# Kernel tuning notes

Measured on AMD Instinct MI355X. Metric: run time of the kernel, lower is better.

## Reference

```python
import jax, jax.numpy as jnp
import numpy as np

NEG_INF = -1e30


def setup_inputs() -> dict:
    key = jax.random.key(0)
    k1, k2, k3, k4 = jax.random.split(key, 4)
    B, T, C, H = 4, 4096, 1024, 64
    x = jax.random.normal(k1, (B, T, C), dtype=jnp.float32)
    Wk = jax.random.normal(k2, (C, H), dtype=jnp.float32) * (C ** -0.5)
    Wq = jax.random.normal(k3, (C, H), dtype=jnp.float32) * (C ** -0.5)
    Wv = jax.random.normal(k4, (C, H), dtype=jnp.float32) * (C ** -0.5)
    return {"x": x, "Wk": Wk, "Wq": Wq, "Wv": Wv}


def reference(x, Wk, Wq, Wv):
    # x: [B, T, C]; Wq/Wk/Wv: [C, H]
    B, T, C = x.shape
    q = jnp.einsum('btc,ch->bth', x, Wq)  # [B,T,H]
    k = jnp.einsum('btc,ch->bth', x, Wk)  # [B,T,H]
    v = jnp.einsum('btc,ch->bth', x, Wv)  # [B,T,H]
    # NOTE: original scales by C**-0.5 (n_embd), not head_size**-0.5.
    scale = jnp.asarray(C, x.dtype) ** -0.5
    wei = jnp.einsum('bth,bsh->bts', q, k) * scale  # [B,T,T]
    causal = jnp.tril(jnp.ones((T, T), dtype=bool))
    wei = jnp.where(causal, wei, NEG_INF)
    wei = jax.nn.softmax(wei, axis=-1)
    # dropout p=0.0 -> identity
    out = jnp.einsum('bts,bsh->bth', wei, v)  # [B,T,H]
    return out
```

## Files before the change

kernel.cpp:

```cpp
#include <hip/hip_runtime.h>
#include <math.h>

typedef short bfx8 __attribute__((ext_vector_type(8)));
typedef short bfx4 __attribute__((ext_vector_type(4)));
typedef float fx4  __attribute__((ext_vector_type(4)));

__device__ __forceinline__ unsigned short f2bf(float f) {
    unsigned int u = __builtin_bit_cast(unsigned int, f);
    u += 0x7FFFu + ((u >> 16) & 1u);
    return (unsigned short)(u >> 16);
}

__global__ __launch_bounds__(256) void wt_prep(const float* __restrict__ Wq,
                                               const float* __restrict__ Wk,
                                               const float* __restrict__ Wv,
                                               unsigned short* __restrict__ wt)
{
    const int k0  = blockIdx.x * 64;
    const int mat = blockIdx.y;
    const float* W = (mat == 0) ? Wq : ((mat == 1) ? Wk : Wv);
    const float scale = (mat == 0) ? 0.03125f : 1.0f;
    __shared__ unsigned short Ls[64 * 68];
    const int t = threadIdx.x;
    #pragma unroll
    for (int i = 0; i < 4; ++i) {
        int idx4 = t + 256 * i;
        int r = idx4 >> 4, c4 = idx4 & 15;
        float4 v = *(const float4*)&W[(size_t)(k0 + r) * 64 + c4 * 4];
        Ls[r * 68 + c4 * 4 + 0] = f2bf(v.x * scale);
        Ls[r * 68 + c4 * 4 + 1] = f2bf(v.y * scale);
        Ls[r * 68 + c4 * 4 + 2] = f2bf(v.z * scale);
        Ls[r * 68 + c4 * 4 + 3] = f2bf(v.w * scale);
    }
    __syncthreads();
    #pragma unroll
    for (int i = 0; i < 2; ++i) {
        int u = t + 256 * i;
        int n = u >> 3, kc = u & 7;
        bfx8 o;
        #pragma unroll
        for (int j = 0; j < 8; ++j) o[j] = (short)Ls[(kc * 8 + j) * 68 + n];
        *(bfx8*)&wt[(size_t)(mat * 64 + n) * 1024 + k0 + kc * 8] = o;
    }
}

__global__ __launch_bounds__(256) void qkv_mfma(
    const float* __restrict__ x, const unsigned short* __restrict__ wt,
    unsigned short* __restrict__ qb, unsigned short* __restrict__ kb,
    unsigned short* __restrict__ vt)
{
    __shared__ alignas(16) char smem[65536];
    const int t = threadIdx.x;
    const int w = t >> 6, l = t & 63, g = l >> 4, li = l & 15;
    const int m0 = blockIdx.x * 64;

    fx4 acc[12];
    #pragma unroll
    for (int i = 0; i < 12; ++i) acc[i] = (fx4){0.f, 0.f, 0.f, 0.f};

    float4 xr[4]; bfx8 wr[6];

#define QKV_LOAD(K0) do { \
    _Pragma("unroll") for (int i_ = 0; i_ < 4; ++i_) { int idx4 = t + 256 * i_; int r_ = idx4 >> 4, c4 = idx4 & 15; \
        xr[i_] = *(const float4*)&x[(size_t)(m0 + r_) * 1024 + (K0) + c4 * 4]; } \
    _Pragma("unroll") for (int i_ = 0; i_ < 6; ++i_) { int idx = t + 256 * i_; int n_ = idx >> 3, c_ = idx & 7; \
        wr[i_] = *(const bfx8*)&wt[(size_t)n_ * 1024 + (K0) + c_ * 8]; } \
} while (0)

#define QKV_STORE(BI) do { \
    char* xb_ = smem + ((BI) ? 8192 : 0); \
    char* wb_ = smem + 16384 + ((BI) ? 24576 : 0); \
    _Pragma("unroll") for (int i_ = 0; i_ < 4; ++i_) { int idx4 = t + 256 * i_; int r_ = idx4 >> 4, c4 = idx4 & 15; \
        bfx4 o_; o_[0] = (short)f2bf(xr[i_].x); o_[1] = (short)f2bf(xr[i_].y); \
        o_[2] = (short)f2bf(xr[i_].z); o_[3] = (short)f2bf(xr[i_].w); \
        *(bfx4*)(xb_ + ((r_ * 128 + c4 * 8) ^ ((r_ & 7) << 4))) = o_; } \
    _Pragma("unroll") for (int i_ = 0; i_ < 6; ++i_) { int idx = t + 256 * i_; int n_ = idx >> 3, c_ = idx & 7; \
        *(bfx8*)(wb_ + ((n_ * 128 + c_ * 16) ^ ((n_ & 7) << 4))) = wr[i_]; } \
} while (0)

    QKV_LOAD(0); QKV_STORE(0);
    __syncthreads();

    for (int ch = 0; ch < 16; ++ch) {
        if (ch + 1 < 16) QKV_LOAD((ch + 1) * 64);
        if (ch) __syncthreads();
        char* xb = smem + ((ch & 1) ? 8192 : 0);
        char* wb = smem + 16384 + ((ch & 1) ? 24576 : 0);
        const int arow = w * 16 + li;
        #pragma unroll
        for (int kk = 0; kk < 2; ++kk) {
            bfx8 af = *(bfx8*)(xb + ((arow * 128 + kk * 64 + g * 16) ^ ((arow & 7) << 4)));
            #pragma unroll
            for (int nb = 0; nb < 12; ++nb) {
                int nrow = nb * 16 + li;
                bfx8 bf = *(bfx8*)(wb + ((nrow * 128 + kk * 64 + g * 16) ^ ((nrow & 7) << 4)));
                acc[nb] = __builtin_amdgcn_mfma_f32_16x16x32_bf16(af, bf, acc[nb], 0, 0, 0);
            }
        }
        if (ch + 1 < 16) QKV_STORE((ch + 1) & 1);
    }

    const int mrow = m0 + w * 16 + g * 4;
    #pragma unroll
    for (int nb = 0; nb < 4; ++nb)
        #pragma unroll
        for (int r = 0; r < 4; ++r)
            qb[(size_t)(mrow + r) * 64 + nb * 16 + li] = f2bf(acc[nb][r]);
    #pragma unroll
    for (int nb = 4; nb < 8; ++nb)
        #pragma unroll
        for (int r = 0; r < 4; ++r)
            kb[(size_t)(mrow + r) * 64 + (nb - 4) * 16 + li] = f2bf(acc[nb][r]);

    __syncthreads();
    unsigned short* Vt = (unsigned short*)smem;
    #pragma unroll
    for (int nb = 8; nb < 12; ++nb)
        #pragma unroll
        for (int r = 0; r < 4; ++r)
            Vt[((nb - 8) * 16 + li) * 64 + (w * 16 + g * 4 + r)] = f2bf(acc[nb][r]);
    __syncthreads();
    const int bb = m0 >> 12, mt = m0 & 4095;
    #pragma unroll
    for (int i = 0; i < 2; ++i) {
        int idx = t + 256 * i;
        int d = idx >> 3, c = idx & 7;
        *(bfx8*)&vt[((size_t)(bb * 64 + d)) * 4096 + mt + c * 8] = *(bfx8*)&Vt[d * 64 + c * 8];
    }
}

__global__ __launch_bounds__(256) void attn_mfma(
    const unsigned short* __restrict__ qb, const unsigned short* __restrict__ kb,
    const unsigned short* __restrict__ vt, float* __restrict__ out)
{
    __shared__ alignas(16) char smem[69632];
    const int t = threadIdx.x;
    const int w = t >> 6, l = t & 63, g = l >> 4, li = l & 15;
    const int bx = blockIdx.x;
    const int b  = bx & 3;
    const int qt = 127 - (bx >> 2);
    const int qbase = qt * 32;
    const int qsub = w & 1, par = w >> 1;

    const unsigned short* Qg = qb + (size_t)b * 4096 * 64;
    const unsigned short* Kg = kb + (size_t)b * 4096 * 64;
    const unsigned short* Vg = vt + (size_t)b * 64 * 4096;

    const int nch = (qbase + 32 + 127) >> 7;

    bfx8 krg[4], vrg[4];

#define ATT_LOAD(CB) do { \
    _Pragma("unroll") for (int i_ = 0; i_ < 4; ++i_) { int idx = t + 256 * i_; int r_ = idx >> 3, c_ = idx & 7; \
        krg[i_] = *(const bfx8*)&Kg[(size_t)((CB) + r_) * 64 + c_ * 8]; } \
    _Pragma("unroll") for (int i_ = 0; i_ < 4; ++i_) { int idx = t + 256 * i_; int d_ = idx >> 4, c_ = idx & 15; \
        vrg[i_] = *(const bfx8*)&Vg[(size_t)d_ * 4096 + (CB) + c_ * 8]; } \
} while (0)

#define ATT_STORE(BI) do { \
    char* kb_ = smem + 4096 + ((BI) ? 16384 : 0); \
    char* vb_ = smem + 36864 + ((BI) ? 16384 : 0); \
    _Pragma("unroll") for (int i_ = 0; i_ < 4; ++i_) { int idx = t + 256 * i_; int r_ = idx >> 3, c_ = idx & 7; \
        *(bfx8*)(kb_ + ((r_ * 128 + c_ * 16) ^ ((r_ & 7) << 4))) = krg[i_]; } \
    _Pragma("unroll") for (int i_ = 0; i_ < 4; ++i_) { int idx = t + 256 * i_; int d_ = idx >> 4, c_ = idx & 15; \
        *(bfx8*)(vb_ + ((d_ * 256 + c_ * 16) ^ ((d_ & 7) << 4))) = vrg[i_]; } \
} while (0)

    {
        int r2 = t >> 3, c2 = t & 7;
        bfx8 qv = *(const bfx8*)&Qg[(size_t)(qbase + r2) * 64 + c2 * 8];
        *(bfx8*)(smem + ((r2 * 128 + c2 * 16) ^ ((r2 & 7) << 4))) = qv;
    }
    ATT_LOAD(0); ATT_STORE(0);
    __syncthreads();

    const int qrow  = qsub * 16 + li;
    const int qglob = qbase + qrow;
    const bfx8 qf0 = *(bfx8*)(smem + ((qrow * 128 + g * 16)      ^ ((qrow & 7) << 4)));
    const bfx8 qf1 = *(bfx8*)(smem + ((qrow * 128 + 64 + g * 16) ^ ((qrow & 7) << 4)));
    const int qmaxr = qbase + qsub * 16 + 15;

    fx4 o[4];
    #pragma unroll
    for (int i = 0; i < 4; ++i) o[i] = (fx4){0.f, 0.f, 0.f, 0.f};
    float m = -1e30f, lsum = 0.f;

    for (int ch = 0; ch < nch; ++ch) {
        const int cb = ch << 7;
        if (ch + 1 < nch) ATT_LOAD(cb + 128);
        if (ch) __syncthreads();
        char* ks = smem + 4096  + ((ch & 1) ? 16384 : 0);
        char* vs = smem + 36864 + ((ch & 1) ? 16384 : 0);
        const int sub = cb + par * 64;
        if (sub <= qmaxr) {
            fx4 s[4];
            #pragma unroll
            for (int i = 0; i < 4; ++i) s[i] = (fx4){0.f, 0.f, 0.f, 0.f};
            #pragma unroll
            for (int st = 0; st < 4; ++st) {
                int krow = par * 64 + st * 16 + li;
                int sw = (krow & 7) << 4;
                bfx8 kf0 = *(bfx8*)(ks + ((krow * 128 + g * 16)      ^ sw));
                bfx8 kf1 = *(bfx8*)(ks + ((krow * 128 + 64 + g * 16) ^ sw));
                s[st] = __builtin_amdgcn_mfma_f32_16x16x32_bf16(kf0, qf0, s[st], 0, 0, 0);
                s[st] = __builtin_amdgcn_mfma_f32_16x16x32_bf16(kf1, qf1, s[st], 0, 0, 0);
            }
            float p[16]; float pmax = -1e30f;
            #pragma unroll
            for (int st = 0; st < 4; ++st)
                #pragma unroll
                for (int rr = 0; rr < 4; ++rr) {
                    int kv = sub + st * 16 + 4 * g + rr;
                    float vvv = (kv <= qglob) ? s[st][rr] : -1e30f;
                    p[st * 4 + rr] = vvv;
                    pmax = fmaxf(pmax, vvv);
                }
            pmax = fmaxf(pmax, __shfl_xor(pmax, 16));
            pmax = fmaxf(pmax, __shfl_xor(pmax, 32));
            if (__any(pmax > m + 8.f)) {
                float mnew = fmaxf(m, pmax);
                float fac = __expf(m - mnew);
                m = mnew; lsum *= fac;
                #pragma unroll
                for (int d2 = 0; d2 < 4; ++d2) {
                    o[d2][0] *= fac; o[d2][1] *= fac; o[d2][2] *= fac; o[d2][3] *= fac;
                }
            }
            float ps = 0.f;
            #pragma unroll
            for (int e = 0; e < 16; ++e) { p[e] = __expf(p[e] - m); ps += p[e]; }
            ps += __shfl_xor(ps, 16);
            ps += __shfl_xor(ps, 32);
            lsum += ps;
            bfx8 pf0, pf1;
            #pragma unroll
            for (int e = 0; e < 8; ++e) { pf0[e] = (short)f2bf(p[e]); pf1[e] = (short)f2bf(p[8 + e]); }
            #pragma unroll
            for (int dblk = 0; dblk < 4; ++dblk) {
                int dr = dblk * 16 + li;
                int base = dr * 256 + par * 128;
                int sw = (dr & 7) << 4;
                bfx4 a0 = *(bfx4*)(vs + ((base + 8 * g)      ^ sw));
                bfx4 a1 = *(bfx4*)(vs + ((base + 32 + 8 * g) ^ sw));
                bfx8 vf0;
                vf0[0] = a0[0]; vf0[1] = a0[1]; vf0[2] = a0[2]; vf0[3] = a0[3];
                vf0[4] = a1[0]; vf0[5] = a1[1]; vf0[6] = a1[2]; vf0[7] = a1[3];
                o[dblk] = __builtin_amdgcn_mfma_f32_16x16x32_bf16(vf0, pf0, o[dblk], 0, 0, 0);
                bfx4 b0 = *(bfx4*)(vs + ((base + 64 + 8 * g) ^ sw));
                bfx4 b1 = *(bfx4*)(vs + ((base + 96 + 8 * g) ^ sw));
                bfx8 vf1;
                vf1[0] = b0[0]; vf1[1] = b0[1]; vf1[2] = b0[2]; vf1[3] = b0[3];
                vf1[4] = b1[0]; vf1[5] = b1[1]; vf1[6] = b1[2]; vf1[7] = b1[3];
                o[dblk] = __builtin_amdgcn_mfma_f32_16x16x32_bf16(vf1, pf1, o[dblk], 0, 0, 0);
            }
        }
        if (ch + 1 < nch) ATT_STORE((ch + 1) & 1);
    }

    __syncthreads();
    float* Osh = (float*)(smem + 4096);
    float* msh = (float*)smem;
    #pragma unroll
    for (int dblk = 0; dblk < 4; ++dblk)
        #pragma unroll
        for (int r = 0; r < 4; ++r)
            Osh[(w * 16 + li) * 64 + dblk * 16 + g * 4 + r] = o[dblk][r];
    if (g == 0) { msh[w * 16 + li] = m; msh[64 + w * 16 + li] = lsum; }
    __syncthreads();

    const int q = t >> 3, dc = (t & 7) * 8;
    const int ql = q & 15, qs2 = q >> 4;
    const int wA = qs2, wB = qs2 + 2;
    const float mA = msh[wA * 16 + ql], mB = msh[wB * 16 + ql];
    const float lA = msh[64 + wA * 16 + ql], lB = msh[64 + wB * 16 + ql];
    const float M  = fmaxf(mA, mB);
    const float eA = __expf(mA - M), eB = __expf(mB - M);
    const float inv = 1.f / (lA * eA + lB * eB);
    float* orow = out + ((size_t)b * 4096 + qbase + q) * 64 + dc;
    const float* OA = &Osh[(wA * 16 + ql) * 64 + dc];
    const float* OB = &Osh[(wB * 16 + ql) * 64 + dc];
    #pragma unroll
    for (int j = 0; j < 8; ++j)
        orow[j] = (OA[j] * eA + OB[j] * eB) * inv;
}

extern "C" void kernel_launch(void* const* d_in, const int* in_sizes, int n_in,
                              void* d_out, int out_size, void* d_ws, size_t ws_size,
                              hipStream_t stream)
{
    const float* x  = (const float*)d_in[0];
    const float* Wk = (const float*)d_in[1];
    const float* Wq = (const float*)d_in[2];
    const float* Wv = (const float*)d_in[3];
    float* outp = (float*)d_out;

    unsigned short* qbuf = (unsigned short*)d_ws;
    unsigned short* kbuf = qbuf + (1u << 20);
    unsigned short* vtb  = kbuf + (1u << 20);
    unsigned short* wtb  = vtb  + (1u << 20);

    wt_prep<<<dim3(16, 3), 256, 0, stream>>>(Wq, Wk, Wv, wtb);
    qkv_mfma<<<256, 256, 0, stream>>>(x, wtb, qbuf, kbuf, vtb);
    attn_mfma<<<512, 256, 0, stream>>>(qbuf, kbuf, vtb, outp);
}
```

Baseline: 70.18 us.

## Software-pipeline QK^T across chunks, use exp2 softmax, and split QKV projection finer

The attention loop is restructured so the QK^T MFMAs for the next K chunk are issued before the softmax and PV of the current chunk. K is prefetched two chunks ahead and V one chunk ahead, with s_setprio raised around the MFMA blocks. log2(e) is folded into the Q scale so the softmax uses exp2f, and the per-lane row-sum shuffles are replaced by shared-memory partial sums reduced in the epilogue. Unmasked tiles now skip the causal mask, and output stores are vectorised. The QKV projection uses 32-row tiles over 512 blocks for more parallelism, at the cost of loading the weight tile twice as often per row of x.

```diff
diff --git a/kernel.cpp b/kernel.cpp
--- a/kernel.cpp
+++ b/kernel.cpp
@@ -9,6 +9,13 @@
     unsigned int u = __builtin_bit_cast(unsigned int, f);
     u += 0x7FFFu + ((u >> 16) & 1u);
     return (unsigned short)(u >> 16);
+}
+
+__device__ __forceinline__ short2 pk_bf16(float a, float b) {
+    short2 r;
+    r.x = (short)f2bf(a);
+    r.y = (short)f2bf(b);
+    return r;
 }
 
 __global__ __launch_bounds__(256) void wt_prep(const float* __restrict__ Wq,
@@ -19,7 +26,7 @@
     const int k0  = blockIdx.x * 64;
     const int mat = blockIdx.y;
     const float* W = (mat == 0) ? Wq : ((mat == 1) ? Wk : Wv);
-    const float scale = (mat == 0) ? 0.03125f : 1.0f;
+    const float scale = (mat == 0) ? (0.03125f * 1.4426950408889634f) : 1.0f;
     __shared__ unsigned short Ls[64 * 68];
     const int t = threadIdx.x;
     #pragma unroll
@@ -49,30 +56,32 @@
     unsigned short* __restrict__ qb, unsigned short* __restrict__ kb,
     unsigned short* __restrict__ vt)
 {
-    __shared__ alignas(16) char smem[65536];
+    __shared__ alignas(16) char smem[57344];
     const int t = threadIdx.x;
     const int w = t >> 6, l = t & 63, g = l >> 4, li = l & 15;
-    const int m0 = blockIdx.x * 64;
-
-    fx4 acc[12];
-    #pragma unroll
-    for (int i = 0; i < 12; ++i) acc[i] = (fx4){0.f, 0.f, 0.f, 0.f};
-
-    float4 xr[4]; bfx8 wr[6];
+    const int m0 = blockIdx.x * 32;
+    const int rh  = (w & 1) * 16;
+    const int nb0 = (w >> 1) * 6;
+
+    fx4 acc[6];
+    #pragma unroll
+    for (int i = 0; i < 6; ++i) acc[i] = (fx4){0.f, 0.f, 0.f, 0.f};
+
+    float4 xr[2]; bfx8 wr[6];
 
 #define QKV_LOAD(K0) do { \
-    _Pragma("unroll") for (int i_ = 0; i_ < 4; ++i_) { int idx4 = t + 256 * i_; int r_ = idx4 >> 4, c4 = idx4 & 15; \
+    _Pragma("unroll") for (int i_ = 0; i_ < 2; ++i_) { int idx4 = t + 256 * i_; int r_ = idx4 >> 4, c4 = idx4 & 15; \
         xr[i_] = *(const float4*)&x[(size_t)(m0 + r_) * 1024 + (K0) + c4 * 4]; } \
     _Pragma("unroll") for (int i_ = 0; i_ < 6; ++i_) { int idx = t + 256 * i_; int n_ = idx >> 3, c_ = idx & 7; \
         wr[i_] = *(const bfx8*)&wt[(size_t)n_ * 1024 + (K0) + c_ * 8]; } \
 } while (0)
 
 #define QKV_STORE(BI) do { \
-    char* xb_ = smem + ((BI) ? 8192 : 0); \
-    char* wb_ = smem + 16384 + ((BI) ? 24576 : 0); \
-    _Pragma("unroll") for (int i_ = 0; i_ < 4; ++i_) { int idx4 = t + 256 * i_; int r_ = idx4 >> 4, c4 = idx4 & 15; \
-        bfx4 o_; o_[0] = (short)f2bf(xr[i_].x); o_[1] = (short)f2bf(xr[i_].y); \
-        o_[2] = (short)f2bf(xr[i_].z); o_[3] = (short)f2bf(xr[i_].w); \
+    char* xb_ = smem + (BI) * 4096; \
+    char* wb_ = smem + 8192 + (BI) * 24576; \
+    _Pragma("unroll") for (int i_ = 0; i_ < 2; ++i_) { int idx4 = t + 256 * i_; int r_ = idx4 >> 4, c4 = idx4 & 15; \
+        short2 lo_ = pk_bf16(xr[i_].x, xr[i_].y), hi_ = pk_bf16(xr[i_].z, xr[i_].w); \
+        bfx4 o_; o_[0] = lo_.x; o_[1] = lo_.y; o_[2] = hi_.x; o_[3] = hi_.y; \
         *(bfx4*)(xb_ + ((r_ * 128 + c4 * 8) ^ ((r_ & 7) << 4))) = o_; } \
     _Pragma("unroll") for (int i_ = 0; i_ < 6; ++i_) { int idx = t + 256 * i_; int n_ = idx >> 3, c_ = idx & 7; \
         *(bfx8*)(wb_ + ((n_ * 128 + c_ * 16) ^ ((n_ & 7) << 4))) = wr[i_]; } \
@@ -84,15 +93,15 @@
     for (int ch = 0; ch < 16; ++ch) {
         if (ch + 1 < 16) QKV_LOAD((ch + 1) * 64);
         if (ch) __syncthreads();
-        char* xb = smem + ((ch & 1) ? 8192 : 0);
-        char* wb = smem + 16384 + ((ch & 1) ? 24576 : 0);
-        const int arow = w * 16 + li;
+        char* xb = smem + (ch & 1) * 4096;
+        char* wb = smem + 8192 + (ch & 1) * 24576;
+        const int arow = rh + li;
         #pragma unroll
         for (int kk = 0; kk < 2; ++kk) {
             bfx8 af = *(bfx8*)(xb + ((arow * 128 + kk * 64 + g * 16) ^ ((arow & 7) << 4)));
             #pragma unroll
-            for (int nb = 0; nb < 12; ++nb) {
-                int nrow = nb * 16 + li;
+            for (int nb = 0; nb < 6; ++nb) {
+                int nrow = (nb0 + nb) * 16 + li;
                 bfx8 bf = *(bfx8*)(wb + ((nrow * 128 + kk * 64 + g * 16) ^ ((nrow & 7) << 4)));
                 acc[nb] = __builtin_amdgcn_mfma_f32_16x16x32_bf16(af, bf, acc[nb], 0, 0, 0);
             }
@@ -100,32 +109,37 @@
         if (ch + 1 < 16) QKV_STORE((ch + 1) & 1);
     }
 
-    const int mrow = m0 + w * 16 + g * 4;
-    #pragma unroll
-    for (int nb = 0; nb < 4; ++nb)
-        #pragma unroll
-        for (int r = 0; r < 4; ++r)
-            qb[(size_t)(mrow + r) * 64 + nb * 16 + li] = f2bf(acc[nb][r]);
-    #pragma unroll
-    for (int nb = 4; nb < 8; ++nb)
-        #pragma unroll
-        for (int r = 0; r < 4; ++r)
-            kb[(size_t)(mrow + r) * 64 + (nb - 4) * 16 + li] = f2bf(acc[nb][r]);
+    const int mrow = m0 + rh + g * 4;
+    #pragma unroll
+    for (int nb = 0; nb < 6; ++nb) {
+        const int nbg = nb0 + nb;
+        if (nbg < 4) {
+            #pragma unroll
+            for (int r = 0; r < 4; ++r)
+                qb[(size_t)(mrow + r) * 64 + nbg * 16 + li] = f2bf(acc[nb][r]);
+        } else if (nbg < 8) {
+            #pragma unroll
+            for (int r = 0; r < 4; ++r)
+                kb[(size_t)(mrow + r) * 64 + (nbg - 4) * 16 + li] = f2bf(acc[nb][r]);
+        }
+    }
 
     __syncthreads();
     unsigned short* Vt = (unsigned short*)smem;
     #pragma unroll
-    for (int nb = 8; nb < 12; ++nb)
-        #pragma unroll
-        for (int r = 0; r < 4; ++r)
-            Vt[((nb - 8) * 16 + li) * 64 + (w * 16 + g * 4 + r)] = f2bf(acc[nb][r]);
+    for (int nb = 0; nb < 6; ++nb) {
+        const int nbg = nb0 + nb;
+        if (nbg >= 8) {
+            #pragma unroll
+            for (int r = 0; r < 4; ++r)
+                Vt[((nbg - 8) * 16 + li) * 40 + rh + g * 4 + r] = f2bf(acc[nb][r]);
+        }
+    }
     __syncthreads();
     const int bb = m0 >> 12, mt = m0 & 4095;
-    #pragma unroll
-    for (int i = 0; i < 2; ++i) {
-        int idx = t + 256 * i;
-        int d = idx >> 3, c = idx & 7;
-        *(bfx8*)&vt[((size_t)(bb * 64 + d)) * 4096 + mt + c * 8] = *(bfx8*)&Vt[d * 64 + c * 8];
+    {
+        int d = t >> 2, c = t & 3;
+        *(bfx8*)&vt[((size_t)(bb * 64 + d)) * 4096 + mt + c * 8] = *(bfx8*)&Vt[d * 40 + c * 8];
     }
 }
 
@@ -145,23 +159,25 @@
     const unsigned short* Qg = qb + (size_t)b * 4096 * 64;
     const unsigned short* Kg = kb + (size_t)b * 4096 * 64;
     const unsigned short* Vg = vt + (size_t)b * 64 * 4096;
-
     const int nch = (qbase + 32 + 127) >> 7;
 
     bfx8 krg[4], vrg[4];
 
-#define ATT_LOAD(CB) do { \
+#define ATT_LOAD_K(CB) do { \
     _Pragma("unroll") for (int i_ = 0; i_ < 4; ++i_) { int idx = t + 256 * i_; int r_ = idx >> 3, c_ = idx & 7; \
         krg[i_] = *(const bfx8*)&Kg[(size_t)((CB) + r_) * 64 + c_ * 8]; } \
+} while (0)
+#define ATT_LOAD_V(CB) do { \
     _Pragma("unroll") for (int i_ = 0; i_ < 4; ++i_) { int idx = t + 256 * i_; int d_ = idx >> 4, c_ = idx & 15; \
         vrg[i_] = *(const bfx8*)&Vg[(size_t)d_ * 4096 + (CB) + c_ * 8]; } \
 } while (0)
-
-#define ATT_STORE(BI) do { \
-    char* kb_ = smem + 4096 + ((BI) ? 16384 : 0); \
-    char* vb_ = smem + 36864 + ((BI) ? 16384 : 0); \
+#define ATT_STORE_K(BI) do { \
+    char* kb_ = smem + 4096 + (BI) * 16384; \
     _Pragma("unroll") for (int i_ = 0; i_ < 4; ++i_) { int idx = t + 256 * i_; int r_ = idx >> 3, c_ = idx & 7; \
         *(bfx8*)(kb_ + ((r_ * 128 + c_ * 16) ^ ((r_ & 7) << 4))) = krg[i_]; } \
+} while (0)
+#define ATT_STORE_V(BI) do { \
+    char* vb_ = smem + 36864 + (BI) * 16384; \
     _Pragma("unroll") for (int i_ = 0; i_ < 4; ++i_) { int idx = t + 256 * i_; int d_ = idx >> 4, c_ = idx & 15; \
         *(bfx8*)(vb_ + ((d_ * 256 + c_ * 16) ^ ((d_ & 7) << 4))) = vrg[i_]; } \
 } while (0)
@@ -171,117 +187,145 @@
         bfx8 qv = *(const bfx8*)&Qg[(size_t)(qbase + r2) * 64 + c2 * 8];
         *(bfx8*)(smem + ((r2 * 128 + c2 * 16) ^ ((r2 & 7) << 4))) = qv;
     }
-    ATT_LOAD(0); ATT_STORE(0);
+    ATT_LOAD_K(0); ATT_LOAD_V(0);
+    ATT_STORE_K(0); ATT_STORE_V(0);
+    if (nch > 1) { ATT_LOAD_K(128); ATT_STORE_K(1); }
     __syncthreads();
 
     const int qrow  = qsub * 16 + li;
     const int qglob = qbase + qrow;
+    const int qmin  = qbase + qsub * 16;
+    const int qmaxr = qmin + 15;
     const bfx8 qf0 = *(bfx8*)(smem + ((qrow * 128 + g * 16)      ^ ((qrow & 7) << 4)));
     const bfx8 qf1 = *(bfx8*)(smem + ((qrow * 128 + 64 + g * 16) ^ ((qrow & 7) << 4)));
-    const int qmaxr = qbase + qsub * 16 + 15;
 
     fx4 o[4];
     #pragma unroll
     for (int i = 0; i < 4; ++i) o[i] = (fx4){0.f, 0.f, 0.f, 0.f};
     float m = -1e30f, lsum = 0.f;
-
-    for (int ch = 0; ch < nch; ++ch) {
-        const int cb = ch << 7;
-        if (ch + 1 < nch) ATT_LOAD(cb + 128);
-        if (ch) __syncthreads();
-        char* ks = smem + 4096  + ((ch & 1) ? 16384 : 0);
-        char* vs = smem + 36864 + ((ch & 1) ? 16384 : 0);
-        const int sub = cb + par * 64;
-        if (sub <= qmaxr) {
-            fx4 s[4];
-            #pragma unroll
-            for (int i = 0; i < 4; ++i) s[i] = (fx4){0.f, 0.f, 0.f, 0.f};
-            #pragma unroll
-            for (int st = 0; st < 4; ++st) {
-                int krow = par * 64 + st * 16 + li;
-                int sw = (krow & 7) << 4;
-                bfx8 kf0 = *(bfx8*)(ks + ((krow * 128 + g * 16)      ^ sw));
-                bfx8 kf1 = *(bfx8*)(ks + ((krow * 128 + 64 + g * 16) ^ sw));
-                s[st] = __builtin_amdgcn_mfma_f32_16x16x32_bf16(kf0, qf0, s[st], 0, 0, 0);
-                s[st] = __builtin_amdgcn_mfma_f32_16x16x32_bf16(kf1, qf1, s[st], 0, 0, 0);
-            }
-            float p[16]; float pmax = -1e30f;
-            #pragma unroll
-            for (int st = 0; st < 4; ++st)
-                #pragma unroll
-                for (int rr = 0; rr < 4; ++rr) {
-                    int kv = sub + st * 16 + 4 * g + rr;
-                    float vvv = (kv <= qglob) ? s[st][rr] : -1e30f;
-                    p[st * 4 + rr] = vvv;
-                    pmax = fmaxf(pmax, vvv);
-                }
-            pmax = fmaxf(pmax, __shfl_xor(pmax, 16));
-            pmax = fmaxf(pmax, __shfl_xor(pmax, 32));
-            if (__any(pmax > m + 8.f)) {
-                float mnew = fmaxf(m, pmax);
-                float fac = __expf(m - mnew);
-                m = mnew; lsum *= fac;
-                #pragma unroll
-                for (int d2 = 0; d2 < 4; ++d2) {
-                    o[d2][0] *= fac; o[d2][1] *= fac; o[d2][2] *= fac; o[d2][3] *= fac;
-                }
-            }
-            float ps = 0.f;
-            #pragma unroll
-            for (int e = 0; e < 16; ++e) { p[e] = __expf(p[e] - m); ps += p[e]; }
-            ps += __shfl_xor(ps, 16);
-            ps += __shfl_xor(ps, 32);
-            lsum += ps;
-            bfx8 pf0, pf1;
-            #pragma unroll
-            for (int e = 0; e < 8; ++e) { pf0[e] = (short)f2bf(p[e]); pf1[e] = (short)f2bf(p[8 + e]); }
-            #pragma unroll
-            for (int dblk = 0; dblk < 4; ++dblk) {
-                int dr = dblk * 16 + li;
-                int base = dr * 256 + par * 128;
-                int sw = (dr & 7) << 4;
-                bfx4 a0 = *(bfx4*)(vs + ((base + 8 * g)      ^ sw));
-                bfx4 a1 = *(bfx4*)(vs + ((base + 32 + 8 * g) ^ sw));
-                bfx8 vf0;
-                vf0[0] = a0[0]; vf0[1] = a0[1]; vf0[2] = a0[2]; vf0[3] = a0[3];
-                vf0[4] = a1[0]; vf0[5] = a1[1]; vf0[6] = a1[2]; vf0[7] = a1[3];
-                o[dblk] = __builtin_amdgcn_mfma_f32_16x16x32_bf16(vf0, pf0, o[dblk], 0, 0, 0);
-                bfx4 b0 = *(bfx4*)(vs + ((base + 64 + 8 * g) ^ sw));
-                bfx4 b1 = *(bfx4*)(vs + ((base + 96 + 8 * g) ^ sw));
-                bfx8 vf1;
-                vf1[0] = b0[0]; vf1[1] = b0[1]; vf1[2] = b0[2]; vf1[3] = b0[3];
-                vf1[4] = b1[0]; vf1[5] = b1[1]; vf1[6] = b1[2]; vf1[7] = b1[3];
-                o[dblk] = __builtin_amdgcn_mfma_f32_16x16x32_bf16(vf1, pf1, o[dblk], 0, 0, 0);
-            }
-        }
-        if (ch + 1 < nch) ATT_STORE((ch + 1) & 1);
-    }
-
-    __syncthreads();
+    fx4 sA[4], sB[4];
+    #pragma unroll
+    for (int i = 0; i < 4; ++i) { sA[i] = (fx4){0.f,0.f,0.f,0.f}; sB[i] = (fx4){0.f,0.f,0.f,0.f}; }
+
+#define QKT(SN, KSB) do { \
+    SN[0] = SN[1] = SN[2] = SN[3] = (fx4){0.f, 0.f, 0.f, 0.f}; \
+    __builtin_amdgcn_s_setprio(1); \
+    _Pragma("unroll") for (int st_ = 0; st_ < 4; ++st_) { \
+        int krow_ = par * 64 + st_ * 16 + li; int sw_ = (krow_ & 7) << 4; \
+        bfx8 kf0_ = *(bfx8*)((KSB) + ((krow_ * 128 + g * 16) ^ sw_)); \
+        bfx8 kf1_ = *(bfx8*)((KSB) + ((krow_ * 128 + 64 + g * 16) ^ sw_)); \
+        SN[st_] = __builtin_amdgcn_mfma_f32_16x16x32_bf16(kf0_, qf0, SN[st_], 0, 0, 0); \
+        SN[st_] = __builtin_amdgcn_mfma_f32_16x16x32_bf16(kf1_, qf1, SN[st_], 0, 0, 0); } \
+    __builtin_amdgcn_s_setprio(0); \
+} while (0)
+
+#define BODY(CUR, NXT, CH) do { \
+    const int cb_ = (CH) << 7; \
+    const bool ldK_ = (CH) + 2 < nch; \
+    const bool ldV_ = (CH) + 1 < nch; \
+    if (ldK_) ATT_LOAD_K(cb_ + 256); \
+    if (ldV_) ATT_LOAD_V(cb_ + 128); \
+    if (((CH) + 1 < nch) && (cb_ + 128 + par * 64 <= qmaxr)) \
+        QKT(NXT, smem + 4096 + ((((CH) + 1) & 1) * 16384)); \
+    if (cb_ + par * 64 <= qmaxr) { \
+        const int sub_ = cb_ + par * 64; \
+        float p[16]; \
+        if (sub_ + 63 > qmin) {   \
+            _Pragma("unroll") for (int st_ = 0; st_ < 4; ++st_) \
+            _Pragma("unroll") for (int rr_ = 0; rr_ < 4; ++rr_) { \
+                int kv_ = sub_ + st_ * 16 + 4 * g + rr_; \
+                p[st_ * 4 + rr_] = (kv_ <= qglob) ? CUR[st_][rr_] : -1e30f; } \
+        } else { \
+            _Pragma("unroll") for (int st_ = 0; st_ < 4; ++st_) \
+            _Pragma("unroll") for (int rr_ = 0; rr_ < 4; ++rr_) \
+                p[st_ * 4 + rr_] = CUR[st_][rr_]; \
+        } \
+        float x0_ = fmaxf(fmaxf(p[0], p[1]),  fmaxf(p[2], p[3])); \
+        float x1_ = fmaxf(fmaxf(p[4], p[5]),  fmaxf(p[6], p[7])); \
+        float x2_ = fmaxf(fmaxf(p[8], p[9]),  fmaxf(p[10], p[11])); \
+        float x3_ = fmaxf(fmaxf(p[12], p[13]), fmaxf(p[14], p[15])); \
+        float pmax_ = fmaxf(fmaxf(x0_, x1_), fmaxf(x2_, x3_)); \
+        pmax_ = fmaxf(pmax_, __shfl_xor(pmax_, 16)); \
+        pmax_ = fmaxf(pmax_, __shfl_xor(pmax_, 32)); \
+        if (__any(pmax_ > m + 8.f)) {   \
+            float mnew_ = fmaxf(m, pmax_); \
+            float fac_ = exp2f(m - mnew_); \
+            m = mnew_; lsum *= fac_; \
+            _Pragma("unroll") for (int d2_ = 0; d2_ < 4; ++d2_) { \
+                o[d2_][0] *= fac_; o[d2_][1] *= fac_; o[d2_][2] *= fac_; o[d2_][3] *= fac_; } } \
+        _Pragma("unroll") for (int e_ = 0; e_ < 16; ++e_) p[e_] = exp2f(p[e_] - m); \
+        lsum += (((p[0]+p[1])+(p[2]+p[3])) + ((p[4]+p[5])+(p[6]+p[7]))) \
+              + (((p[8]+p[9])+(p[10]+p[11])) + ((p[12]+p[13])+(p[14]+p[15]))); \
+        bfx8 pf0_, pf1_; \
+        _Pragma("unroll") for (int i_ = 0; i_ < 4; ++i_) { \
+            short2 a_ = pk_bf16(p[2*i_], p[2*i_+1]);       pf0_[2*i_] = a_.x; pf0_[2*i_+1] = a_.y; \
+            short2 b_ = pk_bf16(p[8+2*i_], p[8+2*i_+1]);   pf1_[2*i_] = b_.x; pf1_[2*i_+1] = b_.y; } \
+        char* vs_ = smem + 36864 + (((CH) & 1) * 16384); \
+        __builtin_amdgcn_s_setprio(1); \
+        _Pragma("unroll") for (int dblk_ = 0; dblk_ < 4; ++dblk_) { \
+            int dr_ = dblk_ * 16 + li; int base_ = dr_ * 256 + par * 128; int sw_ = (dr_ & 7) << 4; \
+            bfx4 a0_ = *(bfx4*)(vs_ + ((base_ + 8 * g) ^ sw_)); \
+            bfx4 a1_ = *(bfx4*)(vs_ + ((base_ + 32 + 8 * g) ^ sw_)); \
+            bfx8 vf_; vf_[0]=a0_[0]; vf_[1]=a0_[1]; vf_[2]=a0_[2]; vf_[3]=a0_[3]; \
+                      vf_[4]=a1_[0]; vf_[5]=a1_[1]; vf_[6]=a1_[2]; vf_[7]=a1_[3]; \
+            o[dblk_] = __builtin_amdgcn_mfma_f32_16x16x32_bf16(vf_, pf0_, o[dblk_], 0, 0, 0); \
+            bfx4 b0_ = *(bfx4*)(vs_ + ((base_ + 64 + 8 * g) ^ sw_)); \
+            bfx4 b1_ = *(bfx4*)(vs_ + ((base_ + 96 + 8 * g) ^ sw_)); \
+            bfx8 vg_; vg_[0]=b0_[0]; vg_[1]=b0_[1]; vg_[2]=b0_[2]; vg_[3]=b0_[3]; \
+                      vg_[4]=b1_[0]; vg_[5]=b1_[1]; vg_[6]=b1_[2]; vg_[7]=b1_[3]; \
+            o[dblk_] = __builtin_amdgcn_mfma_f32_16x16x32_bf16(vg_, pf1_, o[dblk_], 0, 0, 0); } \
+        __builtin_amdgcn_s_setprio(0); \
+    } \
+    if (ldK_) ATT_STORE_K((CH) & 1); \
+    if (ldV_) ATT_STORE_V(((CH) + 1) & 1); \
+    __syncthreads(); \
+} while (0)
+
+    if (par * 64 <= qmaxr) QKT(sA, smem + 4096);
+    __syncthreads();
+
+    int ch = 0;
+    for (; ch + 1 < nch; ch += 2) {
+        BODY(sA, sB, ch);
+        BODY(sB, sA, ch + 1);
+    }
+    if (ch < nch) BODY(sA, sB, ch);
+
     float* Osh = (float*)(smem + 4096);
     float* msh = (float*)smem;
+    float* lsh = (float*)(smem + 1024);
     #pragma unroll
     for (int dblk = 0; dblk < 4; ++dblk)
         #pragma unroll
         for (int r = 0; r < 4; ++r)
             Osh[(w * 16 + li) * 64 + dblk * 16 + g * 4 + r] = o[dblk][r];
-    if (g == 0) { msh[w * 16 + li] = m; msh[64 + w * 16 + li] = lsum; }
+    if (g == 0) msh[w * 16 + li] = m;
+    lsh[(w * 4 + g) * 16 + li] = lsum;
     __syncthreads();
 
     const int q = t >> 3, dc = (t & 7) * 8;
     const int ql = q & 15, qs2 = q >> 4;
     const int wA = qs2, wB = qs2 + 2;
     const float mA = msh[wA * 16 + ql], mB = msh[wB * 16 + ql];
-    const float lA = msh[64 + wA * 16 + ql], lB = msh[64 + wB * 16 + ql];
+    const float lA = lsh[(wA * 4 + 0) * 16 + ql] + lsh[(wA * 4 + 1) * 16 + ql]
+                   + lsh[(wA * 4 + 2) * 16 + ql] + lsh[(wA * 4 + 3) * 16 + ql];
+    const float lB = lsh[(wB * 4 + 0) * 16 + ql] + lsh[(wB * 4 + 1) * 16 + ql]
+                   + lsh[(wB * 4 + 2) * 16 + ql] + lsh[(wB * 4 + 3) * 16 + ql];
     const float M  = fmaxf(mA, mB);
-    const float eA = __expf(mA - M), eB = __expf(mB - M);
+    const float eA = exp2f(mA - M), eB = exp2f(mB - M);
     const float inv = 1.f / (lA * eA + lB * eB);
     float* orow = out + ((size_t)b * 4096 + qbase + q) * 64 + dc;
     const float* OA = &Osh[(wA * 16 + ql) * 64 + dc];
     const float* OB = &Osh[(wB * 16 + ql) * 64 + dc];
-    #pragma unroll
-    for (int j = 0; j < 8; ++j)
-        orow[j] = (OA[j] * eA + OB[j] * eB) * inv;
+    float4 ra0 = *(const float4*)&OA[0], ra1 = *(const float4*)&OA[4];
+    float4 rb0 = *(const float4*)&OB[0], rb1 = *(const float4*)&OB[4];
+    float4 r0, r1;
+    r0.x = (ra0.x * eA + rb0.x * eB) * inv; r0.y = (ra0.y * eA + rb0.y * eB) * inv;
+    r0.z = (ra0.z * eA + rb0.z * eB) * inv; r0.w = (ra0.w * eA + rb0.w * eB) * inv;
+    r1.x = (ra1.x * eA + rb1.x * eB) * inv; r1.y = (ra1.y * eA + rb1.y * eB) * inv;
+    r1.z = (ra1.z * eA + rb1.z * eB) * inv; r1.w = (ra1.w * eA + rb1.w * eB) * inv;
+    *(float4*)&orow[0] = r0;
+    *(float4*)&orow[4] = r1;
 }
 
 extern "C" void kernel_launch(void* const* d_in, const int* in_sizes, int n_in,
@@ -300,6 +344,6 @@
     unsigned short* wtb  = vtb  + (1u << 20);
 
     wt_prep<<<dim3(16, 3), 256, 0, stream>>>(Wq, Wk, Wv, wtb);
-    qkv_mfma<<<256, 256, 0, stream>>>(x, wtb, qbuf, kbuf, vtb);
+    qkv_mfma<<<512, 256, 0, stream>>>(x, wtb, qbuf, kbuf, vtb);
     attn_mfma<<<512, 256, 0, stream>>>(qbuf, kbuf, vtb, outp);
 }
```

Result: no change. 70.49 us, median of 2 (+0.4%).
